# Optimization experiments

Measured on AMD Instinct MI355X. Metric: run time of the kernel, lower is better.

Reference implementation:

```python
import jax, jax.numpy as jnp
import numpy as np

B, C, H, W = 16, 512, 32, 32
EPS = 1e-5

def setup_inputs() -> dict:
    key = jax.random.key(0)
    ks = jax.random.split(key, 7)
    s = 1.0 / np.sqrt(C)
    return {
        "x": jax.random.normal(ks[0], (B, C, H, W), dtype=jnp.float32),
        "norm_w": jnp.ones((C,), jnp.float32),
        "norm_b": jnp.zeros((C,), jnp.float32),
        "qkv_w": jax.random.normal(ks[1], (3 * C, C), dtype=jnp.float32) * s,
        "qkv_b": jax.random.normal(ks[2], (3 * C,), dtype=jnp.float32) * 0.01,
        "out_w": jax.random.normal(ks[3], (C, C), dtype=jnp.float32) * s,
        "out_b": jax.random.normal(ks[4], (C,), dtype=jnp.float32) * 0.01,
    }

def reference(x, norm_w, norm_b, qkv_w, qkv_b, out_w, out_b):
    b, c, h, w = x.shape
    # GroupNorm with num_groups=1: normalize over (C,H,W) per sample, per-channel affine
    mean = jnp.mean(x, axis=(1, 2, 3), keepdims=True)
    var = jnp.var(x, axis=(1, 2, 3), keepdims=True)
    xn = (x - mean) * jax.lax.rsqrt(var + EPS)
    xn = xn * norm_w[None, :, None, None] + norm_b[None, :, None, None]
    # 1x1 conv QKV: [b,3c,h,w]
    qkv = jnp.einsum('bchw,oc->bohw', xn, qkv_w) + qkv_b[None, :, None, None]
    q, k, v = jnp.split(qkv, 3, axis=1)
    n = h * w
    q = q.transpose(0, 2, 3, 1).reshape(b, n, c)   # [b, N, c]
    k = k.reshape(b, c, n)                          # [b, c, N]
    v = v.transpose(0, 2, 3, 1).reshape(b, n, c)   # [b, N, c]
    scores = jnp.einsum('bnc,bcm->bnm', q, k) * (c ** -0.5)  # [b, N, N]
    attn = jax.nn.softmax(scores, axis=-1)
    out = jnp.einsum('bnm,bmc->bnc', attn, v)       # [b, N, c]
    out = out.reshape(b, h, w, c).transpose(0, 3, 1, 2)
    out = jnp.einsum('bchw,oc->bohw', out, out_w) + out_b[None, :, None, None]
    return out + x
```

## Files before the change

### kernel.cpp

```cpp
#include <hip/hip_runtime.h>
#include <math.h>

#define BATCH 16
#define CH    512
#define NTOK  1024
#define CHW   (CH * NTOK)
#define EPSV  1e-5f

typedef __attribute__((ext_vector_type(8))) short bf16x8;
typedef __attribute__((ext_vector_type(4))) float f32x4;

__device__ __forceinline__ unsigned short f2bf(float f) {
    union { float f; unsigned u; } cv; cv.f = f;
    unsigned r = cv.u + 0x7FFFu + ((cv.u >> 16) & 1u);
    return (unsigned short)(r >> 16);
}
__device__ __forceinline__ float bf2f(unsigned short u) {
    union { unsigned u; float f; } cv; cv.u = ((unsigned)u) << 16;
    return cv.f;
}

__device__ __forceinline__ void async16(const unsigned short* g, unsigned short* l) {
    __builtin_amdgcn_global_load_lds(
        (const __attribute__((address_space(1))) void*)g,
        (__attribute__((address_space(3))) void*)l,
        16, 0, 0);
}

static const size_t OFF_WQKV = 256;
static const size_t OFF_OW   = OFF_WQKV + 1572864;
static const size_t OFF_XNT  = OFF_OW   + 524288;
static const size_t OFF_QT   = OFF_XNT  + 16777216;
static const size_t OFF_KT   = OFF_QT   + 16777216;
static const size_t OFF_V    = OFF_KT   + 16777216;
static const size_t OFF_OT   = OFF_V    + 16777216;

__global__ void k_zero_stats(float* ws) {
    if (threadIdx.x < 64) ws[threadIdx.x] = 0.0f;
}

__global__ __launch_bounds__(256) void k_stats_partial(const float* __restrict__ x, float* __restrict__ ws) {
    int blk   = blockIdx.x;
    int b     = blk >> 6;
    int chunk = blk & 63;
    const float4* xp = (const float4*)(x + (size_t)b * CHW + (size_t)chunk * 8192);
    int t = threadIdx.x;
    float s = 0.0f, ss = 0.0f;
#pragma unroll
    for (int j = 0; j < 8; j++) {
        float4 v = xp[t + j * 256];
        s  += v.x + v.y + v.z + v.w;
        ss += v.x * v.x + v.y * v.y + v.z * v.z + v.w * v.w;
    }
#pragma unroll
    for (int off = 32; off; off >>= 1) {
        s  += __shfl_xor(s, off, 64);
        ss += __shfl_xor(ss, off, 64);
    }
    __shared__ float ls[4], lss[4];
    int wave = t >> 6, lane = t & 63;
    if (lane == 0) { ls[wave] = s; lss[wave] = ss; }
    __syncthreads();
    if (t == 0) {
        atomicAdd(&ws[b], ls[0] + ls[1] + ls[2] + ls[3]);
        atomicAdd(&ws[16 + b], lss[0] + lss[1] + lss[2] + lss[3]);
    }
}

__global__ void k_stats_final(float* ws) {
    int b = threadIdx.x;
    if (b < 16) {
        float inv  = 1.0f / (float)CHW;
        float mean = ws[b] * inv;
        float var  = ws[16 + b] * inv - mean * mean;
        ws[32 + b] = mean;
        ws[48 + b] = rsqrtf(var + EPSV);
    }
}

__global__ __launch_bounds__(256) void k_cvt2(const float* __restrict__ wq, const float* __restrict__ wo,
                                              unsigned short* __restrict__ WQ, unsigned short* __restrict__ WO) {
    int i = blockIdx.x * 256 + threadIdx.x;
    const float* src; unsigned short* dst; int off;
    if (i < 196608) { src = wq; dst = WQ; off = i; }
    else            { src = wo; dst = WO; off = i - 196608; }
    float4 v = ((const float4*)src)[off];
    ushort4 o;
    o.x = f2bf(v.x); o.y = f2bf(v.y); o.z = f2bf(v.z); o.w = f2bf(v.w);
    ((ushort4*)dst)[off] = o;
}

__global__ __launch_bounds__(256) void k_xnt(const float* __restrict__ x,
                                             const float* __restrict__ nw,
                                             const float* __restrict__ nb,
                                             const float* __restrict__ ws,
                                             unsigned short* __restrict__ xnt) {
    __shared__ float ls[64][65];
    int b  = blockIdx.z;
    int c0 = blockIdx.y * 64;
    int n0 = blockIdx.x * 64;
    float mean = ws[32 + b], rstd = ws[48 + b];
    int t = threadIdx.x;
    int cl = t >> 4, n4 = t & 15;
    const float* xb = x + (size_t)b * CHW;
#pragma unroll
    for (int i = 0; i < 4; i++) {
        int c = c0 + cl + i * 16;
        float a  = rstd * nw[c];
        float bb = nb[c] - mean * a;
        float4 v = *(const float4*)(xb + (size_t)c * NTOK + n0 + n4 * 4);
        ls[cl + i * 16][n4 * 4 + 0] = v.x * a + bb;
        ls[cl + i * 16][n4 * 4 + 1] = v.y * a + bb;
        ls[cl + i * 16][n4 * 4 + 2] = v.z * a + bb;
        ls[cl + i * 16][n4 * 4 + 3] = v.w * a + bb;
    }
    __syncthreads();
    int nl = t >> 4, c4 = t & 15;
    unsigned short* dst = xnt + (size_t)b * NTOK * CH;
#pragma unroll
    for (int i = 0; i < 4; i++) {
        int n = n0 + nl + i * 16;
        ushort4 o;
        o.x = f2bf(ls[c4 * 4 + 0][nl + i * 16]);
        o.y = f2bf(ls[c4 * 4 + 1][nl + i * 16]);
        o.z = f2bf(ls[c4 * 4 + 2][nl + i * 16]);
        o.w = f2bf(ls[c4 * 4 + 3][nl + i * 16]);
        *(ushort4*)(dst + (size_t)n * CH + c0 + c4 * 4) = o;
    }
}

__device__ __forceinline__ void mfma_core2(const unsigned short* __restrict__ A, int lda,
                                           const unsigned short* __restrict__ B, int ldb,
                                           int K, int m0, int n0,
                                           unsigned short* sm,
                                           f32x4 acc[4][8]) {
    const int t = threadIdx.x;
    const int w = t >> 6, lane = t & 63;
    const int wm = (w & 1) * 64, wn = (w >> 1) * 128;
    const int r16 = lane & 15, quad = lane >> 4;
#pragma unroll
    for (int i = 0; i < 4; i++)
#pragma unroll
        for (int j = 0; j < 8; j++) acc[i][j] = (f32x4){0.f, 0.f, 0.f, 0.f};
    const int sr = lane >> 2;
    const int sk = (lane & 3) * 8;
    const unsigned short* gA0 = A + (size_t)(m0 + w * 32 + sr) * lda + sk;
    const unsigned short* gA1 = gA0 + (size_t)16 * lda;
    const unsigned short* gB0 = B + (size_t)(n0 + w * 64 + sr) * ldb + sk;
    const unsigned short* gB1 = gB0 + (size_t)16 * ldb;
    const unsigned short* gB2 = gB0 + (size_t)32 * ldb;
    const unsigned short* gB3 = gB0 + (size_t)48 * ldb;
    unsigned short* lA0 = sm + (w * 32) * 32;
    unsigned short* lA1 = sm + (w * 32 + 16) * 32;
    unsigned short* lB0 = sm + 8192 + (w * 64) * 32;
    unsigned short* lB1 = lB0 + 16 * 32;
    unsigned short* lB2 = lB0 + 32 * 32;
    unsigned short* lB3 = lB0 + 48 * 32;
    const int T = K >> 5;
    async16(gA0, lA0); async16(gA1, lA1);
    async16(gB0, lB0); async16(gB1, lB1); async16(gB2, lB2); async16(gB3, lB3);
    for (int tt = 0; tt < T; tt++) {
        __syncthreads();
        const int ab = (tt & 1) << 12;
        const int bb = (tt & 1) << 13;
        if (tt + 1 < T) {
            const int nab = ab ^ 4096, nbb = bb ^ 8192;
            const int ko = (tt + 1) << 5;
            async16(gA0 + ko, lA0 + nab); async16(gA1 + ko, lA1 + nab);
            async16(gB0 + ko, lB0 + nbb); async16(gB1 + ko, lB1 + nbb);
            async16(gB2 + ko, lB2 + nbb); async16(gB3 + ko, lB3 + nbb);
        }
        bf16x8 af[4], bfr[8];
#pragma unroll
        for (int i = 0; i < 4; i++) af[i]  = *(const bf16x8*)(sm + ab + (wm + i * 16 + r16) * 32 + quad * 8);
#pragma unroll
        for (int j = 0; j < 8; j++) bfr[j] = *(const bf16x8*)(sm + 8192 + bb + (wn + j * 16 + r16) * 32 + quad * 8);
#pragma unroll
        for (int i = 0; i < 4; i++)
#pragma unroll
            for (int j = 0; j < 8; j++)
                acc[i][j] = __builtin_amdgcn_mfma_f32_16x16x32_bf16(af[i], bfr[j], acc[i][j], 0, 0, 0);
    }
}

#define TS1 136
#define TS2 264

__global__ __launch_bounds__(256, 2) void k_gemm_qkv(const unsigned short* __restrict__ Wq,
                                                     const float* __restrict__ qb,
                                                     const unsigned short* __restrict__ XNT,
                                                     unsigned short* __restrict__ QT,
                                                     unsigned short* __restrict__ KT,
                                                     unsigned short* __restrict__ V) {
    __shared__ __align__(16) unsigned short smem[256 * TS1];
    const int b  = blockIdx.z;
    const int m0 = blockIdx.y * 128;
    const int n0 = blockIdx.x * 256;
    f32x4 acc[4][8];
    mfma_core2(Wq, CH, XNT + (size_t)b * NTOK * CH, CH, CH, m0, n0, smem, acc);
    const int t = threadIdx.x;
    const int w = t >> 6, lane = t & 63;
    const int wm = (w & 1) * 64, wn = (w >> 1) * 128;
    const int r16 = lane & 15, quad = lane >> 4;
    const int region = m0 >> 9;
    __syncthreads();
    if (region < 2) {
#pragma unroll
        for (int i = 0; i < 4; i++) {
            const int ol = wm + i * 16 + quad * 4;
            const int og = m0 + ol;
            const float b0 = qb[og], b1 = qb[og + 1], b2 = qb[og + 2], b3 = qb[og + 3];
#pragma unroll
            for (int j = 0; j < 8; j++) {
                const int nl = wn + j * 16 + r16;
                f32x4 a = acc[i][j];
                ushort4 pk;
                pk.x = f2bf(a[0] + b0); pk.y = f2bf(a[1] + b1);
                pk.z = f2bf(a[2] + b2); pk.w = f2bf(a[3] + b3);
                *(ushort4*)(smem + nl * TS1 + ol) = pk;
            }
        }
        __syncthreads();
        unsigned short* dst = ((region == 0) ? QT : KT) + (size_t)b * NTOK * CH + (size_t)n0 * CH + (m0 & 511);
#pragma unroll
        for (int p = 0; p < 32; p++) {
            const int row = (t >> 5) + p * 8;
            const int seg = (t & 31) * 4;
            *(ushort4*)(dst + (size_t)row * CH + seg) = *(const ushort4*)(smem + row * TS1 + seg);
        }
    } else {
#pragma unroll
        for (int i = 0; i < 4; i++) {
            const int ol = wm + i * 16 + quad * 4;
            const int og = m0 + ol;
#pragma unroll
            for (int j = 0; j < 8; j++) {
                const int nl = wn + j * 16 + r16;
                f32x4 a = acc[i][j];
#pragma unroll
                for (int r = 0; r < 4; r++)
                    smem[(ol + r) * TS2 + nl] = f2bf(a[r] + qb[og + r]);
            }
        }
        __syncthreads();
        unsigned short* dst = V + (size_t)b * CH * NTOK + (size_t)(m0 & 511) * NTOK + n0;
#pragma unroll
        for (int p = 0; p < 32; p++) {
            const int row = (t >> 5) + (p & 15) * 8;
            const int seg = (t & 31) * 4 + (p >> 4) * 128;
            *(ushort4*)(dst + (size_t)row * NTOK + seg) = *(const ushort4*)(smem + row * TS2 + seg);
        }
    }
}

__global__ __launch_bounds__(256, 1) void k_attn(const unsigned short* __restrict__ QT,
                                                 const unsigned short* __restrict__ KTg,
                                                 const unsigned short* __restrict__ Vg,
                                                 unsigned short* __restrict__ OT) {
    __shared__ __align__(16) unsigned short sm[69888];
    unsigned short* smK = sm;
    unsigned short* smV = sm + 32768;
    unsigned short* smP = sm + 65536;

    const int bid = blockIdx.x;
    const int xcd = bid & 7, slot = bid >> 3;
    const int b   = xcd * 2 + (slot & 1);
    const int q0  = (slot >> 1) * 64;

    const int t = threadIdx.x;
    const int w = t >> 6, lane = t & 63;
    const int r16 = lane & 15, quad = lane >> 4;
    const int srow = lane >> 2;
    const int scol = (lane & 3) * 8;

    const unsigned short* Qb = QT  + (size_t)b * NTOK * CH;
    const unsigned short* Kb = KTg + (size_t)b * NTOK * CH;
    const unsigned short* Vb = Vg  + (size_t)b * CH * NTOK;

    bf16x8 qf[16];
    {
        const unsigned short* qrow = Qb + (size_t)(q0 + w * 16 + r16) * CH + quad * 8;
#pragma unroll
        for (int kc = 0; kc < 16; kc++)
            qf[kc] = *(const bf16x8*)(qrow + kc * 32);
    }

    f32x4 accO[32];
#pragma unroll
    for (int j = 0; j < 32; j++) accO[j] = (f32x4){0.f, 0.f, 0.f, 0.f};
    float lsum[4] = {0.f, 0.f, 0.f, 0.f};

    {
#pragma unroll
        for (int ci = 0; ci < 4; ci++) {
            const int ch = w + ci * 4;
            const unsigned short* src = Kb + (size_t)srow * CH + ch * 32 + scol;
            unsigned short* dst = smK + ch * 2048;
#pragma unroll
            for (int r = 0; r < 4; r++)
                async16(src + (size_t)(r * 16) * CH, dst + r * 16 * 32);
        }
    }
    __syncthreads();

    for (int kt = 0; kt < 16; kt++) {
#pragma unroll
        for (int ch = 0; ch < 2; ch++) {
            const unsigned short* src = Vb + (size_t)(w * 128 + srow) * NTOK + kt * 64 + ch * 32 + scol;
            unsigned short* dst = smV + ch * 16384 + (w * 128) * 32;
#pragma unroll
            for (int r = 0; r < 8; r++)
                async16(src + (size_t)(r * 16) * NTOK, dst + r * 16 * 32);
        }
        f32x4 accS[4];
#pragma unroll
        for (int j = 0; j < 4; j++) accS[j] = (f32x4){0.f, 0.f, 0.f, 0.f};
#pragma unroll
        for (int kc = 0; kc < 16; kc++) {
#pragma unroll
            for (int j = 0; j < 4; j++) {
                bf16x8 kf = *(const bf16x8*)(smK + kc * 2048 + (j * 16 + r16) * 32 + quad * 8);
                accS[j] = __builtin_amdgcn_mfma_f32_16x16x32_bf16(qf[kc], kf, accS[j], 0, 0, 0);
            }
        }
        const float scale = 0.044194173824159216f;
#pragma unroll
        for (int j = 0; j < 4; j++) {
#pragma unroll
            for (int r = 0; r < 4; r++) {
                float e = __expf(accS[j][r] * scale);
                lsum[r] += e;
                smP[w * 1088 + (quad * 4 + r) * 68 + j * 16 + r16] = f2bf(e);
            }
        }
        __syncthreads();
        if (kt < 15) {
            const int kt1 = kt + 1;
#pragma unroll
            for (int ci = 0; ci < 4; ci++) {
                const int ch = w + ci * 4;
                const unsigned short* src = Kb + (size_t)(kt1 * 64 + srow) * CH + ch * 32 + scol;
                unsigned short* dst = smK + ch * 2048;
#pragma unroll
                for (int r = 0; r < 4; r++)
                    async16(src + (size_t)(r * 16) * CH, dst + r * 16 * 32);
            }
        }
        bf16x8 pf[2];
#pragma unroll
        for (int kc = 0; kc < 2; kc++)
            pf[kc] = *(const bf16x8*)(smP + w * 1088 + r16 * 68 + kc * 32 + quad * 8);
#pragma unroll
        for (int j = 0; j < 32; j++) {
#pragma unroll
            for (int kc = 0; kc < 2; kc++) {
                bf16x8 vf = *(const bf16x8*)(smV + kc * 16384 + (j * 16 + r16) * 32 + quad * 8);
                accO[j] = __builtin_amdgcn_mfma_f32_16x16x32_bf16(pf[kc], vf, accO[j], 0, 0, 0);
            }
        }
        __syncthreads();
    }

#pragma unroll
    for (int r = 0; r < 4; r++) {
        float v = lsum[r];
        v += __shfl_xor(v, 1, 64);
        v += __shfl_xor(v, 2, 64);
        v += __shfl_xor(v, 4, 64);
        v += __shfl_xor(v, 8, 64);
        lsum[r] = 1.0f / v;
    }
#pragma unroll
    for (int j = 0; j < 32; j++) {
#pragma unroll
        for (int r = 0; r < 4; r++)
            sm[(w * 16 + quad * 4 + r) * 520 + j * 16 + r16] = f2bf(accO[j][r] * lsum[r]);
    }
    __syncthreads();
    unsigned short* dst = OT + (size_t)b * NTOK * CH + (size_t)q0 * CH;
#pragma unroll
    for (int p = 0; p < 32; p++) {
        const int row = (t >> 7) + p * 2;
        const int seg = (t & 127) * 4;
        *(ushort4*)(dst + (size_t)row * CH + seg) = *(const ushort4*)(sm + row * 520 + seg);
    }
}

__global__ __launch_bounds__(256, 2) void k_gemm_out(const unsigned short* __restrict__ OW,
                                                     const float* __restrict__ ob,
                                                     const unsigned short* __restrict__ OT,
                                                     const float* __restrict__ x,
                                                     float* __restrict__ out) {
    __shared__ __align__(16) unsigned short smem[24576];
    const int b  = blockIdx.z;
    const int m0 = blockIdx.y * 128;
    const int n0 = blockIdx.x * 256;
    f32x4 acc[4][8];
    mfma_core2(OW, CH, OT + (size_t)b * NTOK * CH, CH, CH, m0, n0, smem, acc);
    const int t = threadIdx.x;
    const int w = t >> 6, lane = t & 63;
    const int wm = (w & 1) * 64, wn = (w >> 1) * 128;
    const int r16 = lane & 15, quad = lane >> 4;
#pragma unroll
    for (int i = 0; i < 4; i++) {
        const int o0g = m0 + wm + i * 16 + quad * 4;
#pragma unroll
        for (int j = 0; j < 8; j++) {
            const int col = n0 + wn + j * 16 + r16;
            f32x4 a = acc[i][j];
#pragma unroll
            for (int r = 0; r < 4; r++) {
                size_t idx = (size_t)b * CHW + (size_t)(o0g + r) * NTOK + col;
                out[idx] = a[r] + ob[o0g + r] + x[idx];
            }
        }
    }
}

extern "C" void kernel_launch(void* const* d_in, const int* in_sizes, int n_in,
                              void* d_out, int out_size, void* d_ws, size_t ws_size,
                              hipStream_t stream) {
    const float* x      = (const float*)d_in[0];
    const float* norm_w = (const float*)d_in[1];
    const float* norm_b = (const float*)d_in[2];
    const float* qkv_w  = (const float*)d_in[3];
    const float* qkv_b  = (const float*)d_in[4];
    const float* out_w  = (const float*)d_in[5];
    const float* out_b  = (const float*)d_in[6];
    float* out = (float*)d_out;
    char* wsb  = (char*)d_ws;

    float* stats = (float*)wsb;
    unsigned short* WQ  = (unsigned short*)(wsb + OFF_WQKV);
    unsigned short* OW  = (unsigned short*)(wsb + OFF_OW);
    unsigned short* XNT = (unsigned short*)(wsb + OFF_XNT);
    unsigned short* QT  = (unsigned short*)(wsb + OFF_QT);
    unsigned short* KT  = (unsigned short*)(wsb + OFF_KT);
    unsigned short* V   = (unsigned short*)(wsb + OFF_V);
    unsigned short* OT  = (unsigned short*)(wsb + OFF_OT);

    k_zero_stats<<<1, 64, 0, stream>>>(stats);
    k_stats_partial<<<BATCH * 64, 256, 0, stream>>>(x, stats);
    k_stats_final<<<1, 16, 0, stream>>>(stats);
    k_cvt2<<<1024, 256, 0, stream>>>(qkv_w, out_w, WQ, OW);
    k_xnt<<<dim3(NTOK / 64, CH / 64, BATCH), 256, 0, stream>>>(x, norm_w, norm_b, stats, XNT);
    k_gemm_qkv<<<dim3(NTOK / 256, 3 * CH / 128, BATCH), 256, 0, stream>>>(WQ, qkv_b, XNT, QT, KT, V);
    k_attn<<<256, 256, 0, stream>>>(QT, KT, V, OT);
    k_gemm_out<<<dim3(NTOK / 256, CH / 128, BATCH), 256, 0, stream>>>(OW, out_b, OT, x, out);
}
```

Measured before the change: 247.9 us.

## Stream K and V through small double-buffered LDS chunks to fit two blocks per CU

The attention kernel now loads K and V in 128-channel chunks into two ping-pong LDS buffers instead of staging whole 64-token tiles. This cuts shared memory from about 140KB to about 74KB, and launch bounds are raised to two blocks per CU so more waves can hide latency. Each chunk's async load is issued one step ahead of its compute. The cost is many more __syncthreads barriers per tile, and the occupancy gain may be limited by the large accumulator register footprint (128 floats of accO plus the Q fragments).

After: 261.5 us. +5.5%, slower.

```diff
diff --git a/kernel.cpp b/kernel.cpp
--- a/kernel.cpp
+++ b/kernel.cpp
@@ -253,14 +253,14 @@
     }
 }
 
-__global__ __launch_bounds__(256, 1) void k_attn(const unsigned short* __restrict__ QT,
+__global__ __launch_bounds__(256, 2) void k_attn(const unsigned short* __restrict__ QT,
                                                  const unsigned short* __restrict__ KTg,
                                                  const unsigned short* __restrict__ Vg,
                                                  unsigned short* __restrict__ OT) {
-    __shared__ __align__(16) unsigned short sm[69888];
+    __shared__ __align__(16) unsigned short sm[37120];
     unsigned short* smK = sm;
-    unsigned short* smV = sm + 32768;
-    unsigned short* smP = sm + 65536;
+    unsigned short* smV = sm + 16384;
+    unsigned short* smP = sm + 32768;
 
     const int bid = blockIdx.x;
     const int xcd = bid & 7, slot = bid >> 3;
@@ -270,13 +270,16 @@
     const int t = threadIdx.x;
     const int w = t >> 6, lane = t & 63;
     const int r16 = lane & 15, quad = lane >> 4;
-    const int srow = lane >> 2;
-    const int scol = (lane & 3) * 8;
+    const int sr4 = lane >> 2;
+    const int sc8 = (lane & 3) * 8;
 
     const unsigned short* Qb = QT  + (size_t)b * NTOK * CH;
     const unsigned short* Kb = KTg + (size_t)b * NTOK * CH;
     const unsigned short* Vb = Vg  + (size_t)b * CH * NTOK;
 
+    const unsigned short* kSrc = Kb + (size_t)(w * 16 + sr4) * CH + sc8;
+    const unsigned short* vSrc = Vb + (size_t)(w * 32 + sr4) * NTOK + sc8;
+
     bf16x8 qf[16];
     {
         const unsigned short* qrow = Qb + (size_t)(q0 + w * 16 + r16) * CH + quad * 8;
@@ -289,41 +292,45 @@
 #pragma unroll
     for (int j = 0; j < 32; j++) accO[j] = (f32x4){0.f, 0.f, 0.f, 0.f};
     float lsum[4] = {0.f, 0.f, 0.f, 0.f};
-
-    {
-#pragma unroll
-        for (int ci = 0; ci < 4; ci++) {
-            const int ch = w + ci * 4;
-            const unsigned short* src = Kb + (size_t)srow * CH + ch * 32 + scol;
-            unsigned short* dst = smK + ch * 2048;
-#pragma unroll
-            for (int r = 0; r < 4; r++)
-                async16(src + (size_t)(r * 16) * CH, dst + r * 16 * 32);
-        }
-    }
-    __syncthreads();
+    const float scale = 0.044194173824159216f;
+
+#pragma unroll
+    for (int kc = 0; kc < 4; kc++)
+        async16(kSrc + kc * 32, smK + (w * 4 + kc) * 512);
 
     for (int kt = 0; kt < 16; kt++) {
-#pragma unroll
-        for (int ch = 0; ch < 2; ch++) {
-            const unsigned short* src = Vb + (size_t)(w * 128 + srow) * NTOK + kt * 64 + ch * 32 + scol;
-            unsigned short* dst = smV + ch * 16384 + (w * 128) * 32;
-#pragma unroll
-            for (int r = 0; r < 8; r++)
-                async16(src + (size_t)(r * 16) * NTOK, dst + r * 16 * 32);
-        }
+        const size_t ktK = (size_t)kt * 64 * CH;
         f32x4 accS[4];
 #pragma unroll
         for (int j = 0; j < 4; j++) accS[j] = (f32x4){0.f, 0.f, 0.f, 0.f};
 #pragma unroll
-        for (int kc = 0; kc < 16; kc++) {
-#pragma unroll
-            for (int j = 0; j < 4; j++) {
-                bf16x8 kf = *(const bf16x8*)(smK + kc * 2048 + (j * 16 + r16) * 32 + quad * 8);
-                accS[j] = __builtin_amdgcn_mfma_f32_16x16x32_bf16(qf[kc], kf, accS[j], 0, 0, 0);
-            }
-        }
-        const float scale = 0.044194173824159216f;
+        for (int c = 0; c < 4; c++) {
+            __syncthreads();
+            if (c < 3) {
+                unsigned short* dst = smK + (((c + 1) & 1) ? 8192 : 0);
+#pragma unroll
+                for (int kc = 0; kc < 4; kc++)
+                    async16(kSrc + ktK + (c + 1) * 128 + kc * 32, dst + (w * 4 + kc) * 512);
+            } else {
+                unsigned short* dst = smV;
+#pragma unroll
+                for (int i = 0; i < 2; i++)
+#pragma unroll
+                    for (int kk = 0; kk < 2; kk++)
+                        async16(vSrc + (size_t)(i * 16) * NTOK + (size_t)kt * 64 + kk * 32,
+                                dst + ((w * 2 + i) * 2 + kk) * 512);
+            }
+            const unsigned short* kbuf = smK + ((c & 1) ? 8192 : 0);
+#pragma unroll
+            for (int kc = 0; kc < 4; kc++) {
+                bf16x8 q = qf[c * 4 + kc];
+#pragma unroll
+                for (int j = 0; j < 4; j++) {
+                    bf16x8 kf = *(const bf16x8*)(kbuf + (j * 4 + kc) * 512 + r16 * 32 + quad * 8);
+                    accS[j] = __builtin_amdgcn_mfma_f32_16x16x32_bf16(q, kf, accS[j], 0, 0, 0);
+                }
+            }
+        }
 #pragma unroll
         for (int j = 0; j < 4; j++) {
 #pragma unroll
@@ -333,32 +340,37 @@
                 smP[w * 1088 + (quad * 4 + r) * 68 + j * 16 + r16] = f2bf(e);
             }
         }
-        __syncthreads();
-        if (kt < 15) {
-            const int kt1 = kt + 1;
-#pragma unroll
-            for (int ci = 0; ci < 4; ci++) {
-                const int ch = w + ci * 4;
-                const unsigned short* src = Kb + (size_t)(kt1 * 64 + srow) * CH + ch * 32 + scol;
-                unsigned short* dst = smK + ch * 2048;
-#pragma unroll
-                for (int r = 0; r < 4; r++)
-                    async16(src + (size_t)(r * 16) * CH, dst + r * 16 * 32);
-            }
-        }
         bf16x8 pf[2];
 #pragma unroll
-        for (int kc = 0; kc < 2; kc++)
-            pf[kc] = *(const bf16x8*)(smP + w * 1088 + r16 * 68 + kc * 32 + quad * 8);
-#pragma unroll
-        for (int j = 0; j < 32; j++) {
-#pragma unroll
-            for (int kc = 0; kc < 2; kc++) {
-                bf16x8 vf = *(const bf16x8*)(smV + kc * 16384 + (j * 16 + r16) * 32 + quad * 8);
-                accO[j] = __builtin_amdgcn_mfma_f32_16x16x32_bf16(pf[kc], vf, accO[j], 0, 0, 0);
-            }
-        }
-        __syncthreads();
+        for (int v = 0; v < 4; v++) {
+            __syncthreads();
+            if (v < 3) {
+                unsigned short* dst = smV + (((v + 1) & 1) ? 8192 : 0);
+#pragma unroll
+                for (int i = 0; i < 2; i++)
+#pragma unroll
+                    for (int kk = 0; kk < 2; kk++)
+                        async16(vSrc + (size_t)((v + 1) * 128 + i * 16) * NTOK + (size_t)kt * 64 + kk * 32,
+                                dst + ((w * 2 + i) * 2 + kk) * 512);
+            } else if (kt < 15) {
+#pragma unroll
+                for (int kc = 0; kc < 4; kc++)
+                    async16(kSrc + ktK + (size_t)64 * CH + kc * 32, smK + (w * 4 + kc) * 512);
+            }
+            if (v == 0) {
+                pf[0] = *(const bf16x8*)(smP + w * 1088 + r16 * 68 + quad * 8);
+                pf[1] = *(const bf16x8*)(smP + w * 1088 + r16 * 68 + 32 + quad * 8);
+            }
+            const unsigned short* vbuf = smV + ((v & 1) ? 8192 : 0);
+#pragma unroll
+            for (int cj = 0; cj < 8; cj++) {
+#pragma unroll
+                for (int kk = 0; kk < 2; kk++) {
+                    bf16x8 vf = *(const bf16x8*)(vbuf + (cj * 2 + kk) * 512 + r16 * 32 + quad * 8);
+                    accO[v * 8 + cj] = __builtin_amdgcn_mfma_f32_16x16x32_bf16(pf[kk], vf, accO[v * 8 + cj], 0, 0, 0);
+                }
+            }
+        }
     }
 
 #pragma unroll
@@ -370,6 +382,7 @@
         v += __shfl_xor(v, 8, 64);
         lsum[r] = 1.0f / v;
     }
+    __syncthreads();
 #pragma unroll
     for (int j = 0; j < 32; j++) {
 #pragma unroll
```

## Swizzle LDS tiles and repartition PV work across waves by channel

Applied to the files above, without the earlier changes.

Adds an XOR swizzle to the LDS layout of the GEMM core and the attention K/V tiles so that fragment reads avoid bank conflicts. In the attention kernel, the P·V product is repartitioned: each wave now owns a 128-channel slice for all 64 query rows instead of all channels for its own 16 rows. Each V fragment read from LDS is therefore reused across 4 MFMAs. Row sums are exchanged through a small LDS buffer so each wave can normalize all rows, at the cost of an extra barrier and more LDS reads of the P tile.

Result: no change. 252.7 us (+2.0%).

```diff
diff --git a/kernel.cpp b/kernel.cpp
--- a/kernel.cpp
+++ b/kernel.cpp
@@ -26,6 +26,7 @@
         (__attribute__((address_space(3))) void*)l,
         16, 0, 0);
 }
+
 
 static const size_t OFF_WQKV = 256;
 static const size_t OFF_OW   = OFF_WQKV + 1572864;
@@ -143,7 +144,8 @@
 #pragma unroll
         for (int j = 0; j < 8; j++) acc[i][j] = (f32x4){0.f, 0.f, 0.f, 0.f};
     const int sr = lane >> 2;
-    const int sk = (lane & 3) * 8;
+    const int sk = (((lane & 3) ^ ((lane >> 3) & 3))) * 8;
+    const int swz = ((quad ^ (r16 >> 1)) & 3) * 8;
     const unsigned short* gA0 = A + (size_t)(m0 + w * 32 + sr) * lda + sk;
     const unsigned short* gA1 = gA0 + (size_t)16 * lda;
     const unsigned short* gB0 = B + (size_t)(n0 + w * 64 + sr) * ldb + sk;
@@ -172,9 +174,9 @@
         }
         bf16x8 af[4], bfr[8];
 #pragma unroll
-        for (int i = 0; i < 4; i++) af[i]  = *(const bf16x8*)(sm + ab + (wm + i * 16 + r16) * 32 + quad * 8);
-#pragma unroll
-        for (int j = 0; j < 8; j++) bfr[j] = *(const bf16x8*)(sm + 8192 + bb + (wn + j * 16 + r16) * 32 + quad * 8);
+        for (int i = 0; i < 4; i++) af[i]  = *(const bf16x8*)(sm + ab + (wm + i * 16 + r16) * 32 + swz);
+#pragma unroll
+        for (int j = 0; j < 8; j++) bfr[j] = *(const bf16x8*)(sm + 8192 + bb + (wn + j * 16 + r16) * 32 + swz);
 #pragma unroll
         for (int i = 0; i < 4; i++)
 #pragma unroll
@@ -257,10 +259,11 @@
                                                  const unsigned short* __restrict__ KTg,
                                                  const unsigned short* __restrict__ Vg,
                                                  unsigned short* __restrict__ OT) {
-    __shared__ __align__(16) unsigned short sm[69888];
+    __shared__ __align__(16) unsigned short sm[70016];
     unsigned short* smK = sm;
     unsigned short* smV = sm + 32768;
     unsigned short* smP = sm + 65536;
+    float* lsumLDS = (float*)(sm + 69888);
 
     const int bid = blockIdx.x;
     const int xcd = bid & 7, slot = bid >> 3;
@@ -271,7 +274,8 @@
     const int w = t >> 6, lane = t & 63;
     const int r16 = lane & 15, quad = lane >> 4;
     const int srow = lane >> 2;
-    const int scol = (lane & 3) * 8;
+    const int sc   = (((lane & 3) ^ ((lane >> 3) & 3))) * 8;
+    const int swz  = ((quad ^ (r16 >> 1)) & 3) * 8;
 
     const unsigned short* Qb = QT  + (size_t)b * NTOK * CH;
     const unsigned short* Kb = KTg + (size_t)b * NTOK * CH;
@@ -289,73 +293,65 @@
 #pragma unroll
     for (int j = 0; j < 32; j++) accO[j] = (f32x4){0.f, 0.f, 0.f, 0.f};
     float lsum[4] = {0.f, 0.f, 0.f, 0.f};
-
-    {
-#pragma unroll
-        for (int ci = 0; ci < 4; ci++) {
-            const int ch = w + ci * 4;
-            const unsigned short* src = Kb + (size_t)srow * CH + ch * 32 + scol;
-            unsigned short* dst = smK + ch * 2048;
-#pragma unroll
-            for (int r = 0; r < 4; r++)
-                async16(src + (size_t)(r * 16) * CH, dst + r * 16 * 32);
-        }
-    }
+    const float scale = 0.044194173824159216f;
+
+#pragma unroll
+    for (int kc = 0; kc < 16; kc++)
+        async16(Kb + (size_t)(w * 16 + srow) * CH + kc * 32 + sc, smK + (w * 16 + kc) * 512);
     __syncthreads();
 
     for (int kt = 0; kt < 16; kt++) {
-#pragma unroll
-        for (int ch = 0; ch < 2; ch++) {
-            const unsigned short* src = Vb + (size_t)(w * 128 + srow) * NTOK + kt * 64 + ch * 32 + scol;
-            unsigned short* dst = smV + ch * 16384 + (w * 128) * 32;
-#pragma unroll
-            for (int r = 0; r < 8; r++)
-                async16(src + (size_t)(r * 16) * NTOK, dst + r * 16 * 32);
+        {
+            const unsigned short* vbase = Vb + (size_t)kt * 64;
+#pragma unroll
+            for (int cg = 0; cg < 8; cg++)
+#pragma unroll
+                for (int kk = 0; kk < 2; kk++)
+                    async16(vbase + (size_t)(w * 128 + cg * 16 + srow) * NTOK + kk * 32 + sc,
+                            smV + ((w * 8 + cg) * 2 + kk) * 512);
         }
         f32x4 accS[4];
 #pragma unroll
         for (int j = 0; j < 4; j++) accS[j] = (f32x4){0.f, 0.f, 0.f, 0.f};
 #pragma unroll
         for (int kc = 0; kc < 16; kc++) {
+            bf16x8 q = qf[kc];
 #pragma unroll
             for (int j = 0; j < 4; j++) {
-                bf16x8 kf = *(const bf16x8*)(smK + kc * 2048 + (j * 16 + r16) * 32 + quad * 8);
-                accS[j] = __builtin_amdgcn_mfma_f32_16x16x32_bf16(qf[kc], kf, accS[j], 0, 0, 0);
-            }
-        }
-        const float scale = 0.044194173824159216f;
+                bf16x8 kf = *(const bf16x8*)(smK + (j * 16 + kc) * 512 + r16 * 32 + swz);
+                accS[j] = __builtin_amdgcn_mfma_f32_16x16x32_bf16(q, kf, accS[j], 0, 0, 0);
+            }
+        }
 #pragma unroll
         for (int j = 0; j < 4; j++) {
 #pragma unroll
             for (int r = 0; r < 4; r++) {
                 float e = __expf(accS[j][r] * scale);
                 lsum[r] += e;
-                smP[w * 1088 + (quad * 4 + r) * 68 + j * 16 + r16] = f2bf(e);
+                smP[(w * 16 + quad * 4 + r) * 68 + j * 16 + r16] = f2bf(e);
             }
         }
         __syncthreads();
         if (kt < 15) {
-            const int kt1 = kt + 1;
-#pragma unroll
-            for (int ci = 0; ci < 4; ci++) {
-                const int ch = w + ci * 4;
-                const unsigned short* src = Kb + (size_t)(kt1 * 64 + srow) * CH + ch * 32 + scol;
-                unsigned short* dst = smK + ch * 2048;
-#pragma unroll
-                for (int r = 0; r < 4; r++)
-                    async16(src + (size_t)(r * 16) * CH, dst + r * 16 * 32);
-            }
-        }
-        bf16x8 pf[2];
-#pragma unroll
-        for (int kc = 0; kc < 2; kc++)
-            pf[kc] = *(const bf16x8*)(smP + w * 1088 + r16 * 68 + kc * 32 + quad * 8);
-#pragma unroll
-        for (int j = 0; j < 32; j++) {
-#pragma unroll
-            for (int kc = 0; kc < 2; kc++) {
-                bf16x8 vf = *(const bf16x8*)(smV + kc * 16384 + (j * 16 + r16) * 32 + quad * 8);
-                accO[j] = __builtin_amdgcn_mfma_f32_16x16x32_bf16(pf[kc], vf, accO[j], 0, 0, 0);
+            const unsigned short* kbase = Kb + (size_t)(kt + 1) * 64 * CH;
+#pragma unroll
+            for (int kc = 0; kc < 16; kc++)
+                async16(kbase + (size_t)(w * 16 + srow) * CH + kc * 32 + sc, smK + (w * 16 + kc) * 512);
+        }
+        bf16x8 pf[4][2];
+#pragma unroll
+        for (int j = 0; j < 4; j++)
+#pragma unroll
+            for (int kk = 0; kk < 2; kk++)
+                pf[j][kk] = *(const bf16x8*)(smP + (j * 16 + r16) * 68 + kk * 32 + quad * 8);
+#pragma unroll
+        for (int cj = 0; cj < 8; cj++) {
+            bf16x8 vf0 = *(const bf16x8*)(smV + ((w * 8 + cj) * 2 + 0) * 512 + r16 * 32 + swz);
+            bf16x8 vf1 = *(const bf16x8*)(smV + ((w * 8 + cj) * 2 + 1) * 512 + r16 * 32 + swz);
+#pragma unroll
+            for (int j = 0; j < 4; j++) {
+                accO[j * 8 + cj] = __builtin_amdgcn_mfma_f32_16x16x32_bf16(pf[j][0], vf0, accO[j * 8 + cj], 0, 0, 0);
+                accO[j * 8 + cj] = __builtin_amdgcn_mfma_f32_16x16x32_bf16(pf[j][1], vf1, accO[j * 8 + cj], 0, 0, 0);
             }
         }
         __syncthreads();
@@ -368,13 +364,21 @@
         v += __shfl_xor(v, 2, 64);
         v += __shfl_xor(v, 4, 64);
         v += __shfl_xor(v, 8, 64);
-        lsum[r] = 1.0f / v;
-    }
-#pragma unroll
-    for (int j = 0; j < 32; j++) {
-#pragma unroll
-        for (int r = 0; r < 4; r++)
-            sm[(w * 16 + quad * 4 + r) * 520 + j * 16 + r16] = f2bf(accO[j][r] * lsum[r]);
+        if (r16 == 0) lsumLDS[w * 16 + quad * 4 + r] = v;
+    }
+    __syncthreads();
+#pragma unroll
+    for (int j = 0; j < 4; j++) {
+        float iv[4];
+#pragma unroll
+        for (int r = 0; r < 4; r++) iv[r] = 1.0f / lsumLDS[j * 16 + quad * 4 + r];
+#pragma unroll
+        for (int cj = 0; cj < 8; cj++) {
+            f32x4 a = accO[j * 8 + cj];
+#pragma unroll
+            for (int r = 0; r < 4; r++)
+                sm[(j * 16 + quad * 4 + r) * 520 + w * 128 + cj * 16 + r16] = f2bf(a[r] * iv[r]);
+        }
     }
     __syncthreads();
     unsigned short* dst = OT + (size_t)b * NTOK * CH + (size_t)q0 * CH;
```
